# Performance work log

Hardware: AMD Instinct MI355X
Metric: run time of the kernel (lower is better)

The kernel has to match this reference:

```python
import jax, jax.numpy as jnp
import numpy as np


def setup_inputs() -> dict:
    key = jax.random.key(0)
    ks = jax.random.split(key, 6)
    B, S, E, H = 8, 2048, 1024, 64
    scale = 1.0 / np.sqrt(E)
    return {
        "query": jax.random.normal(ks[0], (B, S, E), dtype=jnp.float32),
        "key": jax.random.normal(ks[1], (B, S, E), dtype=jnp.float32),
        "value": jax.random.normal(ks[2], (B, S, E), dtype=jnp.float32),
        "Wq": jax.random.normal(ks[3], (E, H), dtype=jnp.float32) * scale,
        "bq": jnp.zeros((H,), dtype=jnp.float32),
        "Wk": jax.random.normal(ks[4], (E, H), dtype=jnp.float32) * scale,
        "bk": jnp.zeros((H,), dtype=jnp.float32),
        "Wv": jax.random.normal(ks[5], (E, H), dtype=jnp.float32) * scale,
        "bv": jnp.zeros((H,), dtype=jnp.float32),
    }


def reference(query, key, value, Wq, bq, Wk, bk, Wv, bv):
    # Linear projections: [B,S,E] @ [E,H] + [H] -> [B,S,H]
    q = jnp.einsum("bse,eh->bsh", query, Wq) + bq
    k = jnp.einsum("bse,eh->bsh", key, Wk) + bk
    v = jnp.einsum("bse,eh->bsh", value, Wv) + bv
    head_dim = q.shape[-1]
    # scores [B,S,S], softmax over last axis, then weighted sum of values
    scores = jnp.einsum("bqh,bkh->bqk", q, k) / jnp.sqrt(
        jnp.asarray(head_dim, dtype=q.dtype)
    )
    attn = jax.nn.softmax(scores, axis=-1)
    return jnp.einsum("bqk,bkh->bqh", attn, v)
```

## Files before the change

### kernel.cpp

```cpp
#include <hip/hip_runtime.h>
#include <math.h>

#define BB 8
#define SS 2048
#define EE 1024
#define HH 64
#define MM (BB * SS)

typedef unsigned short u16;
typedef __attribute__((ext_vector_type(8))) short short8;
typedef __attribute__((ext_vector_type(4))) float floatx4;

__device__ __forceinline__ u16 f2bf(float f) {
    union { float f; unsigned u; } a; a.f = f;
    unsigned r = a.u + 0x7fffu + ((a.u >> 16) & 1u);
    return (u16)(r >> 16);
}

#define PM 64
#define PK 32

__global__ __launch_bounds__(256) void proj_kernel(
    const float* __restrict__ A0, const float* __restrict__ A1, const float* __restrict__ A2,
    const float* __restrict__ W0, const float* __restrict__ W1, const float* __restrict__ W2,
    const float* __restrict__ b0, const float* __restrict__ b1, const float* __restrict__ b2,
    u16* __restrict__ o0, u16* __restrict__ o1, u16* __restrict__ o2)
{
    const int which = blockIdx.y;
    const float* __restrict__ A    = (which == 0) ? A0 : (which == 1) ? A1 : A2;
    const float* __restrict__ W    = (which == 0) ? W0 : (which == 1) ? W1 : W2;
    const float* __restrict__ bias = (which == 0) ? b0 : (which == 1) ? b1 : b2;
    u16* __restrict__ out          = (which == 0) ? o0 : (which == 1) ? o1 : o2;

    __shared__ __align__(16) float As[PM][PK + 4];
    __shared__ __align__(16) float Ws[PK][HH + 4];

    const int row0 = blockIdx.x * PM;
    const int tid  = threadIdx.x;
    const int tx   = tid & 15;
    const int ty   = tid >> 4;

    float acc[4][4];
    #pragma unroll
    for (int i = 0; i < 4; ++i)
        #pragma unroll
        for (int j = 0; j < 4; ++j) acc[i][j] = 0.f;

    for (int kc = 0; kc < EE; kc += PK) {
        #pragma unroll
        for (int e4 = tid; e4 < PM * PK / 4; e4 += 256) {
            int r = e4 >> 3;
            int c = (e4 & 7) << 2;
            *(float4*)&As[r][c] = *(const float4*)&A[(size_t)(row0 + r) * EE + kc + c];
        }
        #pragma unroll
        for (int e4 = tid; e4 < PK * HH / 4; e4 += 256) {
            int r = e4 >> 4;
            int c = (e4 & 15) << 2;
            *(float4*)&Ws[r][c] = *(const float4*)&W[(size_t)(kc + r) * HH + c];
        }
        __syncthreads();

        #pragma unroll
        for (int kk = 0; kk < PK; ++kk) {
            float a[4];
            #pragma unroll
            for (int i = 0; i < 4; ++i) a[i] = As[ty * 4 + i][kk];
            const float4 w4 = *(const float4*)&Ws[kk][tx * 4];
            #pragma unroll
            for (int i = 0; i < 4; ++i) {
                acc[i][0] = fmaf(a[i], w4.x, acc[i][0]);
                acc[i][1] = fmaf(a[i], w4.y, acc[i][1]);
                acc[i][2] = fmaf(a[i], w4.z, acc[i][2]);
                acc[i][3] = fmaf(a[i], w4.w, acc[i][3]);
            }
        }
        __syncthreads();
    }

    const float4 b4 = *(const float4*)&bias[tx * 4];
    #pragma unroll
    for (int i = 0; i < 4; ++i) {
        ushort4 o;
        o.x = f2bf(acc[i][0] + b4.x);
        o.y = f2bf(acc[i][1] + b4.y);
        o.z = f2bf(acc[i][2] + b4.z);
        o.w = f2bf(acc[i][3] + b4.w);
        *(ushort4*)&out[(size_t)(row0 + ty * 4 + i) * HH + tx * 4] = o;
    }
}

__global__ __launch_bounds__(256) void flash_mfma(
    const u16* __restrict__ qp, const u16* __restrict__ kp,
    const u16* __restrict__ vp, float* __restrict__ out)
{
    __shared__ __align__(16) u16 Ks[128 * 64];
    __shared__ __align__(16) u16 Vt[64 * 128];
    __shared__ __align__(16) u16 Pw[4][16 * 72];

    const int b    = blockIdx.y;
    const int q0   = blockIdx.x * 32;
    const int tid  = threadIdx.x;
    const int lane = tid & 63;
    const int wave = tid >> 6;
    const int wq   = wave & 1;
    const int ks   = wave >> 1;
    const int n    = lane & 15;
    const int g    = lane >> 4;

    const u16* qrow = qp + ((size_t)b * SS + q0 + wq * 16 + n) * HH;
    const short8 qa0 = *(const short8*)(qrow + g * 8);
    const short8 qa1 = *(const short8*)(qrow + 32 + g * 8);

    floatx4 Oa[4];
    #pragma unroll
    for (int ht = 0; ht < 4; ++ht) Oa[ht] = (floatx4){0.f, 0.f, 0.f, 0.f};
    float m_i[4], l_i[4];
    #pragma unroll
    for (int r = 0; r < 4; ++r) { m_i[r] = -1e30f; l_i[r] = 0.f; }

    const u16* kb = kp + (size_t)b * SS * HH;
    const u16* vb = vp + (size_t)b * SS * HH;

    for (int t = 0; t < 16; ++t) {
        __syncthreads();
        #pragma unroll
        for (int it = 0; it < 4; ++it) {
            int c  = it * 256 + tid;
            int j  = c >> 3, cs = c & 7;
            short8 v = *(const short8*)(kb + ((size_t)(t * 128 + j)) * HH + cs * 8);
            *(short8*)&Ks[j * 64 + ((cs ^ (j & 7)) << 3)] = v;
        }
        {
            const int j0 = (tid & 31) * 4, h0 = (tid >> 5) * 8;
            short8 r0 = *(const short8*)(vb + (size_t)(t * 128 + j0 + 0) * HH + h0);
            short8 r1 = *(const short8*)(vb + (size_t)(t * 128 + j0 + 1) * HH + h0);
            short8 r2 = *(const short8*)(vb + (size_t)(t * 128 + j0 + 2) * HH + h0);
            short8 r3 = *(const short8*)(vb + (size_t)(t * 128 + j0 + 3) * HH + h0);
            #pragma unroll
            for (int i = 0; i < 8; ++i) {
                int h = h0 + i;
                ushort4 w;
                w.x = (u16)r0[i]; w.y = (u16)r1[i]; w.z = (u16)r2[i]; w.w = (u16)r3[i];
                *(ushort4*)((char*)Vt + h * 256 + (((j0 >> 3) ^ (h & 7)) << 4) + ((j0 & 4) << 1)) = w;
            }
        }
        __syncthreads();

        floatx4 S[4];
        #pragma unroll
        for (int nt = 0; nt < 4; ++nt) {
            const int j = ks * 64 + nt * 16 + n;
            const short8 kb0 = *(const short8*)&Ks[j * 64 + (((0 + g) ^ (j & 7)) << 3)];
            const short8 kb1 = *(const short8*)&Ks[j * 64 + (((4 + g) ^ (j & 7)) << 3)];
            floatx4 acc = (floatx4){0.f, 0.f, 0.f, 0.f};
            acc = __builtin_amdgcn_mfma_f32_16x16x32_bf16(qa0, kb0, acc, 0, 0, 0);
            acc = __builtin_amdgcn_mfma_f32_16x16x32_bf16(qa1, kb1, acc, 0, 0, 0);
            S[nt] = acc;
        }

        float mx[4];
        #pragma unroll
        for (int r = 0; r < 4; ++r) mx[r] = -1e30f;
        #pragma unroll
        for (int nt = 0; nt < 4; ++nt)
            #pragma unroll
            for (int r = 0; r < 4; ++r) {
                S[nt][r] *= 0.125f;
                mx[r] = fmaxf(mx[r], S[nt][r]);
            }
        #pragma unroll
        for (int off = 8; off >= 1; off >>= 1)
            #pragma unroll
            for (int r = 0; r < 4; ++r)
                mx[r] = fmaxf(mx[r], __shfl_xor(mx[r], off, 64));

        float alpha[4], ps[4];
        #pragma unroll
        for (int r = 0; r < 4; ++r) {
            const float Mn = fmaxf(m_i[r], mx[r]);
            alpha[r] = __expf(m_i[r] - Mn);
            m_i[r]   = Mn;
            ps[r]    = 0.f;
        }
        float p[4][4];
        #pragma unroll
        for (int nt = 0; nt < 4; ++nt)
            #pragma unroll
            for (int r = 0; r < 4; ++r) {
                p[nt][r] = __expf(S[nt][r] - m_i[r]);
                ps[r] += p[nt][r];
            }
        #pragma unroll
        for (int off = 8; off >= 1; off >>= 1)
            #pragma unroll
            for (int r = 0; r < 4; ++r)
                ps[r] += __shfl_xor(ps[r], off, 64);
        #pragma unroll
        for (int r = 0; r < 4; ++r) l_i[r] = l_i[r] * alpha[r] + ps[r];
        #pragma unroll
        for (int ht = 0; ht < 4; ++ht)
            #pragma unroll
            for (int r = 0; r < 4; ++r) Oa[ht][r] *= alpha[r];

        #pragma unroll
        for (int nt = 0; nt < 4; ++nt)
            #pragma unroll
            for (int r = 0; r < 4; ++r)
                Pw[wave][(g * 4 + r) * 72 + nt * 16 + n] = f2bf(p[nt][r]);

        const short8 pa0 = *(const short8*)&Pw[wave][n * 72 + g * 8];
        const short8 pa1 = *(const short8*)&Pw[wave][n * 72 + 32 + g * 8];

        #pragma unroll
        for (int ht = 0; ht < 4; ++ht) {
            const int h = ht * 16 + n;
            const int cj0 = ks * 8 + 0 + g;
            const int cj1 = ks * 8 + 4 + g;
            const short8 vb0 = *(const short8*)((const char*)Vt + h * 256 + ((cj0 ^ (h & 7)) << 4));
            const short8 vb1 = *(const short8*)((const char*)Vt + h * 256 + ((cj1 ^ (h & 7)) << 4));
            Oa[ht] = __builtin_amdgcn_mfma_f32_16x16x32_bf16(pa0, vb0, Oa[ht], 0, 0, 0);
            Oa[ht] = __builtin_amdgcn_mfma_f32_16x16x32_bf16(pa1, vb1, Oa[ht], 0, 0, 0);
        }
    }

    __syncthreads();
    float* Cb = (float*)Ks;
    float* Cm = Cb + 2 * 16 * 68;
    float* Cl = Cm + 32;
    if (ks == 1) {
        #pragma unroll
        for (int ht = 0; ht < 4; ++ht)
            #pragma unroll
            for (int r = 0; r < 4; ++r)
                Cb[(wq * 16 + g * 4 + r) * 68 + ht * 16 + n] = Oa[ht][r];
        if (n == 0)
            #pragma unroll
            for (int r = 0; r < 4; ++r) {
                Cm[wq * 16 + g * 4 + r] = m_i[r];
                Cl[wq * 16 + g * 4 + r] = l_i[r];
            }
    }
    __syncthreads();
    if (ks == 0) {
        float a0[4], a1[4], linv[4];
        #pragma unroll
        for (int r = 0; r < 4; ++r) {
            const int m = g * 4 + r;
            const float m1 = Cm[wq * 16 + m], l1 = Cl[wq * 16 + m];
            const float M  = fmaxf(m_i[r], m1);
            const float e0 = __expf(m_i[r] - M), e1 = __expf(m1 - M);
            a0[r] = e0; a1[r] = e1;
            linv[r] = 1.f / (l_i[r] * e0 + l1 * e1);
        }
        #pragma unroll
        for (int ht = 0; ht < 4; ++ht)
            #pragma unroll
            for (int r = 0; r < 4; ++r) {
                const float o1 = Cb[(wq * 16 + g * 4 + r) * 68 + ht * 16 + n];
                const float v  = (Oa[ht][r] * a0[r] + o1 * a1[r]) * linv[r];
                out[((size_t)b * SS + q0 + wq * 16 + g * 4 + r) * HH + ht * 16 + n] = v;
            }
    }
}

extern "C" void kernel_launch(void* const* d_in, const int* in_sizes, int n_in,
                              void* d_out, int out_size, void* d_ws, size_t ws_size,
                              hipStream_t stream) {
    const float* query = (const float*)d_in[0];
    const float* key   = (const float*)d_in[1];
    const float* value = (const float*)d_in[2];
    const float* Wq    = (const float*)d_in[3];
    const float* bq    = (const float*)d_in[4];
    const float* Wk    = (const float*)d_in[5];
    const float* bk    = (const float*)d_in[6];
    const float* Wv    = (const float*)d_in[7];
    const float* bv    = (const float*)d_in[8];
    float* out = (float*)d_out;

    u16* qp = (u16*)d_ws;
    u16* kp = qp + (size_t)MM * HH;
    u16* vp = kp + (size_t)MM * HH;

    dim3 pgrid(MM / PM, 3);
    proj_kernel<<<pgrid, 256, 0, stream>>>(query, key, value,
                                           Wq, Wk, Wv,
                                           bq, bk, bv,
                                           qp, kp, vp);

    dim3 agrid(SS / 32, BB);
    flash_mfma<<<agrid, 256, 0, stream>>>(qp, kp, vp, out);
}
```

Before: 317.2 us.

## Use split-bf16 MFMA for projections and double-buffer K/V tiles in flash kernel

```diff
diff --git a/kernel.cpp b/kernel.cpp
--- a/kernel.cpp
+++ b/kernel.cpp
@@ -17,10 +17,21 @@
     return (u16)(r >> 16);
 }
 
-#define PM 64
-#define PK 32
-
-__global__ __launch_bounds__(256) void proj_kernel(
+__device__ __forceinline__ void split2(float f0, float f1, unsigned& hp, unsigned& lp) {
+    union { float f; unsigned u; } a0, a1, h0, h1, l0, l1;
+    a0.f = f0; a1.f = f1;
+    h0.u = a0.u & 0xffff0000u;
+    h1.u = a1.u & 0xffff0000u;
+    l0.f = f0 - h0.f;
+    l1.f = f1 - h1.f;
+    hp = __builtin_amdgcn_perm(a1.u, a0.u, 0x07060302u);
+    lp = __builtin_amdgcn_perm(l1.u, l0.u, 0x07060302u);
+}
+
+#define BM 128
+#define BKp 64
+
+__global__ __launch_bounds__(256) void proj_mfma(
     const float* __restrict__ A0, const float* __restrict__ A1, const float* __restrict__ A2,
     const float* __restrict__ W0, const float* __restrict__ W1, const float* __restrict__ W2,
     const float* __restrict__ b0, const float* __restrict__ b1, const float* __restrict__ b2,
@@ -32,70 +43,109 @@
     const float* __restrict__ bias = (which == 0) ? b0 : (which == 1) ? b1 : b2;
     u16* __restrict__ out          = (which == 0) ? o0 : (which == 1) ? o1 : o2;
 
-    __shared__ __align__(16) float As[PM][PK + 4];
-    __shared__ __align__(16) float Ws[PK][HH + 4];
-
-    const int row0 = blockIdx.x * PM;
+    __shared__ __align__(16) u16 Ah[BM][72], Al[BM][72];
+    __shared__ __align__(16) u16 Wh[64][72], Wl[64][72];
+
     const int tid  = threadIdx.x;
-    const int tx   = tid & 15;
-    const int ty   = tid >> 4;
-
-    float acc[4][4];
+    const int lane = tid & 63;
+    const int wave = tid >> 6;
+    const int n    = lane & 15;
+    const int g    = lane >> 4;
+    const int row0 = blockIdx.x * BM;
+
+    const int ar = tid >> 1;
+    const int ak = (tid & 1) * 32;
+    const int wk = (tid >> 4) * 4;
+    const int wn = (tid & 15) * 4;
+
+    floatx4 acc[2][4];
     #pragma unroll
-    for (int i = 0; i < 4; ++i)
-        #pragma unroll
-        for (int j = 0; j < 4; ++j) acc[i][j] = 0.f;
-
-    for (int kc = 0; kc < EE; kc += PK) {
-        #pragma unroll
-        for (int e4 = tid; e4 < PM * PK / 4; e4 += 256) {
-            int r = e4 >> 3;
-            int c = (e4 & 7) << 2;
-            *(float4*)&As[r][c] = *(const float4*)&A[(size_t)(row0 + r) * EE + kc + c];
-        }
-        #pragma unroll
-        for (int e4 = tid; e4 < PK * HH / 4; e4 += 256) {
-            int r = e4 >> 4;
-            int c = (e4 & 15) << 2;
-            *(float4*)&Ws[r][c] = *(const float4*)&W[(size_t)(kc + r) * HH + c];
-        }
+    for (int mt = 0; mt < 2; ++mt)
+        #pragma unroll
+        for (int nt = 0; nt < 4; ++nt) acc[mt][nt] = (floatx4){0.f, 0.f, 0.f, 0.f};
+
+    for (int kc = 0; kc < EE; kc += BKp) {
+        const float* ap = A + (size_t)(row0 + ar) * EE + kc + ak;
+        float4 av[8];
+        #pragma unroll
+        for (int i = 0; i < 8; ++i) av[i] = *(const float4*)(ap + i * 4);
+
         __syncthreads();
 
         #pragma unroll
-        for (int kk = 0; kk < PK; ++kk) {
-            float a[4];
-            #pragma unroll
-            for (int i = 0; i < 4; ++i) a[i] = As[ty * 4 + i][kk];
-            const float4 w4 = *(const float4*)&Ws[kk][tx * 4];
-            #pragma unroll
-            for (int i = 0; i < 4; ++i) {
-                acc[i][0] = fmaf(a[i], w4.x, acc[i][0]);
-                acc[i][1] = fmaf(a[i], w4.y, acc[i][1]);
-                acc[i][2] = fmaf(a[i], w4.z, acc[i][2]);
-                acc[i][3] = fmaf(a[i], w4.w, acc[i][3]);
-            }
+        for (int i = 0; i < 4; ++i) {
+            unsigned hp0, lp0, hp1, lp1, hp2, lp2, hp3, lp3;
+            split2(av[2*i].x,   av[2*i].y,   hp0, lp0);
+            split2(av[2*i].z,   av[2*i].w,   hp1, lp1);
+            split2(av[2*i+1].x, av[2*i+1].y, hp2, lp2);
+            split2(av[2*i+1].z, av[2*i+1].w, hp3, lp3);
+            uint4 h4 = {hp0, hp1, hp2, hp3};
+            uint4 l4 = {lp0, lp1, lp2, lp3};
+            *(uint4*)&Ah[ar][ak + i * 8] = h4;
+            *(uint4*)&Al[ar][ak + i * 8] = l4;
+        }
+
+        float4 wv[4];
+        #pragma unroll
+        for (int i = 0; i < 4; ++i)
+            wv[i] = *(const float4*)&W[(size_t)(kc + wk + i) * HH + wn];
+        #pragma unroll
+        for (int j = 0; j < 4; ++j) {
+            const float e0 = (&wv[0].x)[j], e1 = (&wv[1].x)[j],
+                        e2 = (&wv[2].x)[j], e3 = (&wv[3].x)[j];
+            unsigned hp0, lp0, hp1, lp1;
+            split2(e0, e1, hp0, lp0);
+            split2(e2, e3, hp1, lp1);
+            uint2 h2 = {hp0, hp1};
+            uint2 l2 = {lp0, lp1};
+            *(uint2*)&Wh[wn + j][wk] = h2;
+            *(uint2*)&Wl[wn + j][wk] = l2;
         }
         __syncthreads();
-    }
-
-    const float4 b4 = *(const float4*)&bias[tx * 4];
+
+        #pragma unroll
+        for (int ks = 0; ks < 2; ++ks) {
+            short8 ahf[2], alf[2], whf[4], wlf[4];
+            #pragma unroll
+            for (int mt = 0; mt < 2; ++mt) {
+                ahf[mt] = *(const short8*)&Ah[wave * 32 + mt * 16 + n][ks * 32 + g * 8];
+                alf[mt] = *(const short8*)&Al[wave * 32 + mt * 16 + n][ks * 32 + g * 8];
+            }
+            #pragma unroll
+            for (int nt = 0; nt < 4; ++nt) {
+                whf[nt] = *(const short8*)&Wh[nt * 16 + n][ks * 32 + g * 8];
+                wlf[nt] = *(const short8*)&Wl[nt * 16 + n][ks * 32 + g * 8];
+            }
+            #pragma unroll
+            for (int mt = 0; mt < 2; ++mt)
+                #pragma unroll
+                for (int nt = 0; nt < 4; ++nt) {
+                    acc[mt][nt] = __builtin_amdgcn_mfma_f32_16x16x32_bf16(ahf[mt], whf[nt], acc[mt][nt], 0, 0, 0);
+                    acc[mt][nt] = __builtin_amdgcn_mfma_f32_16x16x32_bf16(alf[mt], whf[nt], acc[mt][nt], 0, 0, 0);
+                    acc[mt][nt] = __builtin_amdgcn_mfma_f32_16x16x32_bf16(ahf[mt], wlf[nt], acc[mt][nt], 0, 0, 0);
+                }
+        }
+    }
+
     #pragma unroll
-    for (int i = 0; i < 4; ++i) {
-        ushort4 o;
-        o.x = f2bf(acc[i][0] + b4.x);
-        o.y = f2bf(acc[i][1] + b4.y);
-        o.z = f2bf(acc[i][2] + b4.z);
-        o.w = f2bf(acc[i][3] + b4.w);
-        *(ushort4*)&out[(size_t)(row0 + ty * 4 + i) * HH + tx * 4] = o;
-    }
+    for (int mt = 0; mt < 2; ++mt)
+        #pragma unroll
+        for (int nt = 0; nt < 4; ++nt) {
+            const float bv = bias[nt * 16 + n];
+            #pragma unroll
+            for (int r = 0; r < 4; ++r) {
+                const int row = row0 + wave * 32 + mt * 16 + g * 4 + r;
+                out[(size_t)row * HH + nt * 16 + n] = f2bf(acc[mt][nt][r] + bv);
+            }
+        }
 }
 
 __global__ __launch_bounds__(256) void flash_mfma(
     const u16* __restrict__ qp, const u16* __restrict__ kp,
     const u16* __restrict__ vp, float* __restrict__ out)
 {
-    __shared__ __align__(16) u16 Ks[128 * 64];
-    __shared__ __align__(16) u16 Vt[64 * 128];
+    __shared__ __align__(16) u16 Ks[2][64 * 64];
+    __shared__ __align__(16) u16 Vt[2][64 * 64];
     __shared__ __align__(16) u16 Pw[4][16 * 72];
 
     const int b    = blockIdx.y;
@@ -122,48 +172,62 @@
     const u16* kb = kp + (size_t)b * SS * HH;
     const u16* vb = vp + (size_t)b * SS * HH;
 
-    for (int t = 0; t < 16; ++t) {
-        __syncthreads();
-        #pragma unroll
-        for (int it = 0; it < 4; ++it) {
-            int c  = it * 256 + tid;
-            int j  = c >> 3, cs = c & 7;
-            short8 v = *(const short8*)(kb + ((size_t)(t * 128 + j)) * HH + cs * 8);
-            *(short8*)&Ks[j * 64 + ((cs ^ (j & 7)) << 3)] = v;
-        }
-        {
-            const int j0 = (tid & 31) * 4, h0 = (tid >> 5) * 8;
-            short8 r0 = *(const short8*)(vb + (size_t)(t * 128 + j0 + 0) * HH + h0);
-            short8 r1 = *(const short8*)(vb + (size_t)(t * 128 + j0 + 1) * HH + h0);
-            short8 r2 = *(const short8*)(vb + (size_t)(t * 128 + j0 + 2) * HH + h0);
-            short8 r3 = *(const short8*)(vb + (size_t)(t * 128 + j0 + 3) * HH + h0);
-            #pragma unroll
-            for (int i = 0; i < 8; ++i) {
-                int h = h0 + i;
-                ushort4 w;
-                w.x = (u16)r0[i]; w.y = (u16)r1[i]; w.z = (u16)r2[i]; w.w = (u16)r3[i];
-                *(ushort4*)((char*)Vt + h * 256 + (((j0 >> 3) ^ (h & 7)) << 4) + ((j0 & 4) << 1)) = w;
-            }
-        }
-        __syncthreads();
-
-        floatx4 S[4];
-        #pragma unroll
-        for (int nt = 0; nt < 4; ++nt) {
-            const int j = ks * 64 + nt * 16 + n;
-            const short8 kb0 = *(const short8*)&Ks[j * 64 + (((0 + g) ^ (j & 7)) << 3)];
-            const short8 kb1 = *(const short8*)&Ks[j * 64 + (((4 + g) ^ (j & 7)) << 3)];
-            floatx4 acc = (floatx4){0.f, 0.f, 0.f, 0.f};
-            acc = __builtin_amdgcn_mfma_f32_16x16x32_bf16(qa0, kb0, acc, 0, 0, 0);
-            acc = __builtin_amdgcn_mfma_f32_16x16x32_bf16(qa1, kb1, acc, 0, 0, 0);
-            S[nt] = acc;
+    const int jK0 = tid >> 3, jK1 = 32 + (tid >> 3), cs = tid & 7;
+    const int jV  = (tid & 15) * 4, hV = (tid >> 4) * 4;
+
+    short8  kr0, kr1;
+    ushort4 vr0, vr1, vr2, vr3;
+
+    kr0 = *(const short8*)(kb + (size_t)jK0 * HH + cs * 8);
+    kr1 = *(const short8*)(kb + (size_t)jK1 * HH + cs * 8);
+    vr0 = *(const ushort4*)(vb + (size_t)(jV + 0) * HH + hV);
+    vr1 = *(const ushort4*)(vb + (size_t)(jV + 1) * HH + hV);
+    vr2 = *(const ushort4*)(vb + (size_t)(jV + 2) * HH + hV);
+    vr3 = *(const ushort4*)(vb + (size_t)(jV + 3) * HH + hV);
+    {
+        *(short8*)&Ks[0][jK0 * 64 + ((cs ^ (jK0 & 7)) << 3)] = kr0;
+        *(short8*)&Ks[0][jK1 * 64 + ((cs ^ (jK1 & 7)) << 3)] = kr1;
+        const u16* a0 = (const u16*)&vr0; const u16* a1 = (const u16*)&vr1;
+        const u16* a2 = (const u16*)&vr2; const u16* a3 = (const u16*)&vr3;
+        #pragma unroll
+        for (int i = 0; i < 4; ++i) {
+            const int h = hV + i;
+            ushort4 w; w.x = a0[i]; w.y = a1[i]; w.z = a2[i]; w.w = a3[i];
+            *(ushort4*)((char*)&Vt[0][0] + h * 128 + (((jV >> 3) ^ (h & 7)) << 4) + ((jV & 4) << 1)) = w;
+        }
+    }
+    __syncthreads();
+
+    for (int t = 0; t < SS / 64; ++t) {
+        const int cur = t & 1;
+
+        if (t + 1 < SS / 64) {
+            const size_t kt = (size_t)(t + 1) * 64;
+            kr0 = *(const short8*)(kb + (kt + jK0) * HH + cs * 8);
+            kr1 = *(const short8*)(kb + (kt + jK1) * HH + cs * 8);
+            vr0 = *(const ushort4*)(vb + (kt + jV + 0) * HH + hV);
+            vr1 = *(const ushort4*)(vb + (kt + jV + 1) * HH + hV);
+            vr2 = *(const ushort4*)(vb + (kt + jV + 2) * HH + hV);
+            vr3 = *(const ushort4*)(vb + (kt + jV + 3) * HH + hV);
+        }
+
+        floatx4 S[2];
+        #pragma unroll
+        for (int nt = 0; nt < 2; ++nt) {
+            const int j = ks * 32 + nt * 16 + n;
+            const short8 kf0 = *(const short8*)&Ks[cur][j * 64 + (((0 + g) ^ (j & 7)) << 3)];
+            const short8 kf1 = *(const short8*)&Ks[cur][j * 64 + (((4 + g) ^ (j & 7)) << 3)];
+            floatx4 a = (floatx4){0.f, 0.f, 0.f, 0.f};
+            a = __builtin_amdgcn_mfma_f32_16x16x32_bf16(qa0, kf0, a, 0, 0, 0);
+            a = __builtin_amdgcn_mfma_f32_16x16x32_bf16(qa1, kf1, a, 0, 0, 0);
+            S[nt] = a;
         }
 
         float mx[4];
         #pragma unroll
         for (int r = 0; r < 4; ++r) mx[r] = -1e30f;
         #pragma unroll
-        for (int nt = 0; nt < 4; ++nt)
+        for (int nt = 0; nt < 2; ++nt)
             #pragma unroll
             for (int r = 0; r < 4; ++r) {
                 S[nt][r] *= 0.125f;
@@ -183,9 +247,9 @@
             m_i[r]   = Mn;
             ps[r]    = 0.f;
         }
-        float p[4][4];
-        #pragma unroll
-        for (int nt = 0; nt < 4; ++nt)
+        float p[2][4];
+        #pragma unroll
+        for (int nt = 0; nt < 2; ++nt)
             #pragma unroll
             for (int r = 0; r < 4; ++r) {
                 p[nt][r] = __expf(S[nt][r] - m_i[r]);
@@ -204,28 +268,37 @@
             for (int r = 0; r < 4; ++r) Oa[ht][r] *= alpha[r];
 
         #pragma unroll
-        for (int nt = 0; nt < 4; ++nt)
+        for (int nt = 0; nt < 2; ++nt)
             #pragma unroll
             for (int r = 0; r < 4; ++r)
                 Pw[wave][(g * 4 + r) * 72 + nt * 16 + n] = f2bf(p[nt][r]);
-
-        const short8 pa0 = *(const short8*)&Pw[wave][n * 72 + g * 8];
-        const short8 pa1 = *(const short8*)&Pw[wave][n * 72 + 32 + g * 8];
+        const short8 pa = *(const short8*)&Pw[wave][n * 72 + g * 8];
 
         #pragma unroll
         for (int ht = 0; ht < 4; ++ht) {
             const int h = ht * 16 + n;
-            const int cj0 = ks * 8 + 0 + g;
-            const int cj1 = ks * 8 + 4 + g;
-            const short8 vb0 = *(const short8*)((const char*)Vt + h * 256 + ((cj0 ^ (h & 7)) << 4));
-            const short8 vb1 = *(const short8*)((const char*)Vt + h * 256 + ((cj1 ^ (h & 7)) << 4));
-            Oa[ht] = __builtin_amdgcn_mfma_f32_16x16x32_bf16(pa0, vb0, Oa[ht], 0, 0, 0);
-            Oa[ht] = __builtin_amdgcn_mfma_f32_16x16x32_bf16(pa1, vb1, Oa[ht], 0, 0, 0);
-        }
-    }
-
-    __syncthreads();
-    float* Cb = (float*)Ks;
+            const short8 vf = *(const short8*)((const char*)&Vt[cur][0] + h * 128 +
+                                               ((((ks << 2) + g) ^ (h & 7)) << 4));
+            Oa[ht] = __builtin_amdgcn_mfma_f32_16x16x32_bf16(pa, vf, Oa[ht], 0, 0, 0);
+        }
+
+        if (t + 1 < SS / 64) {
+            const int nx = cur ^ 1;
+            *(short8*)&Ks[nx][jK0 * 64 + ((cs ^ (jK0 & 7)) << 3)] = kr0;
+            *(short8*)&Ks[nx][jK1 * 64 + ((cs ^ (jK1 & 7)) << 3)] = kr1;
+            const u16* a0 = (const u16*)&vr0; const u16* a1 = (const u16*)&vr1;
+            const u16* a2 = (const u16*)&vr2; const u16* a3 = (const u16*)&vr3;
+            #pragma unroll
+            for (int i = 0; i < 4; ++i) {
+                const int h = hV + i;
+                ushort4 w; w.x = a0[i]; w.y = a1[i]; w.z = a2[i]; w.w = a3[i];
+                *(ushort4*)((char*)&Vt[nx][0] + h * 128 + (((jV >> 3) ^ (h & 7)) << 4) + ((jV & 4) << 1)) = w;
+            }
+        }
+        __syncthreads();
+    }
+
+    float* Cb = (float*)&Ks[0][0];
     float* Cm = Cb + 2 * 16 * 68;
     float* Cl = Cm + 32;
     if (ks == 1) {
@@ -243,14 +316,14 @@
     }
     __syncthreads();
     if (ks == 0) {
-        float a0[4], a1[4], linv[4];
+        float a0v[4], a1v[4], linv[4];
         #pragma unroll
         for (int r = 0; r < 4; ++r) {
             const int m = g * 4 + r;
             const float m1 = Cm[wq * 16 + m], l1 = Cl[wq * 16 + m];
             const float M  = fmaxf(m_i[r], m1);
             const float e0 = __expf(m_i[r] - M), e1 = __expf(m1 - M);
-            a0[r] = e0; a1[r] = e1;
+            a0v[r] = e0; a1v[r] = e1;
             linv[r] = 1.f / (l_i[r] * e0 + l1 * e1);
         }
         #pragma unroll
@@ -258,7 +331,7 @@
             #pragma unroll
             for (int r = 0; r < 4; ++r) {
                 const float o1 = Cb[(wq * 16 + g * 4 + r) * 68 + ht * 16 + n];
-                const float v  = (Oa[ht][r] * a0[r] + o1 * a1[r]) * linv[r];
+                const float v  = (Oa[ht][r] * a0v[r] + o1 * a1v[r]) * linv[r];
                 out[((size_t)b * SS + q0 + wq * 16 + g * 4 + r) * HH + ht * 16 + n] = v;
             }
     }
@@ -282,11 +355,11 @@
     u16* kp = qp + (size_t)MM * HH;
     u16* vp = kp + (size_t)MM * HH;
 
-    dim3 pgrid(MM / PM, 3);
-    proj_kernel<<<pgrid, 256, 0, stream>>>(query, key, value,
-                                           Wq, Wk, Wv,
-                                           bq, bk, bv,
-                                           qp, kp, vp);
+    dim3 pgrid(MM / BM, 3);
+    proj_mfma<<<pgrid, 256, 0, stream>>>(query, key, value,
+                                         Wq, Wk, Wv,
+                                         bq, bk, bv,
+                                         qp, kp, vp);
 
     dim3 agrid(SS / 32, BB);
     flash_mfma<<<agrid, 256, 0, stream>>>(qp, kp, vp, out);
```

Result: faster. 286.4 us (-9.7%).
